# Kernel tuning notes

Hardware: AMD Instinct MI355X
Metric: run time of the kernel (lower is better)

## Reference

```python
import jax, jax.numpy as jnp
import numpy as np

B, N, IN_C, OUT_C = 32, 1024, 64, 128
ALPHA = 0.2  # LeakyReLU negative slope
NEG_INF = -1e16


def setup_inputs() -> dict:
    key = jax.random.key(0)
    k1, k2, k3, k4, k5 = jax.random.split(key, 5)
    inputs = jax.random.normal(k1, (B, N, IN_C), dtype=jnp.float32)
    # dense 0/1 adjacency mask
    graph = jax.random.randint(k2, (N, N), 0, 2).astype(jnp.float32)
    # torch nn.Linear weight layout: [out_c, in_c]
    W = jax.random.normal(k3, (OUT_C, IN_C), dtype=jnp.float32)
    b = jax.random.normal(k4, (OUT_C,), dtype=jnp.float32)
    a = jax.random.normal(k5, (2 * OUT_C, 1), dtype=jnp.float32)
    return {"inputs": inputs, "graph": graph, "W": W, "b": b, "a": a}


def reference(inputs, graph, W, b, a):
    # h = W(inputs): [B, N, D]
    h = jnp.einsum('bnt,dt->bnd', inputs, W)
    # cat([h_i, h_j]) @ a  ==  h_i @ a1 + h_j @ a2  (decomposed, no [B,N,N,2D] tensor)
    a1 = a[:OUT_C, 0]   # [D]
    a2 = a[OUT_C:, 0]   # [D]
    s1 = jnp.einsum('bnd,d->bn', h, a1)  # score contribution of node i
    s2 = jnp.einsum('bnd,d->bn', h, a2)  # score contribution of node j
    e = s1[:, :, None] + s2[:, None, :]  # [B, N, N]
    e = jnp.where(e > 0, e, ALPHA * e)   # LeakyReLU
    e = e * graph                        # zero out non-edges
    # torch masked_fill_(eq(outputs, 0), -1e16)
    e = jnp.where(e == 0.0, NEG_INF, e)
    attention = jax.nn.softmax(e, axis=2)  # [B, N, N]
    out = jnp.einsum('bij,bjd->bid', attention, h) + b  # [B, N, D]
    return out
```

## Files before the change

kernel.cpp:

```cpp
#include <hip/hip_runtime.h>
#include <hip/hip_bf16.h>

#define ALPHA 0.2f

typedef unsigned short ushort_t;
typedef unsigned int   uint_t;
typedef unsigned short ushort8 __attribute__((ext_vector_type(8)));
typedef uint_t uintv4 __attribute__((ext_vector_type(4)));
typedef float f32x4 __attribute__((ext_vector_type(4)));
typedef __bf16 bf16x8 __attribute__((ext_vector_type(8)));

__device__ __forceinline__ ushort_t f2bf(float f) {
  unsigned u = __float_as_uint(f);
  u += 0x7fffu + ((u >> 16) & 1u);
  return (ushort_t)(u >> 16);
}

__global__ __launch_bounds__(256) void gat_pack_kernel(
    const float* __restrict__ graph, const float* __restrict__ W,
    const float* __restrict__ avec, uint_t* __restrict__ gmask,
    float* __restrict__ u)
{
  const int row = blockIdx.x, t = threadIdx.x;
  __shared__ uint_t nibs[256];
  float4 g = ((const float4*)(graph + (size_t)row * 1024))[t];
  uint_t nib = (g.x != 0.f ? 1u : 0u) | (g.y != 0.f ? 2u : 0u) |
               (g.z != 0.f ? 4u : 0u) | (g.w != 0.f ? 8u : 0u);
  nibs[t] = nib;
  __syncthreads();
  if (t < 32) {
    uint_t wd = 0;
#pragma unroll
    for (int k = 0; k < 8; ++k) wd |= nibs[t * 8 + k] << (4 * k);
    gmask[(size_t)row * 32 + t] = wd;
  }
  if (row == 0 && t < 128) {
    const int k  = t & 63;
    const int ao = (t >> 6) * 128;
    float a0 = 0.f, a1 = 0.f, a2 = 0.f, a3 = 0.f;
    for (int d = 0; d < 128; d += 4) {
      a0 = fmaf(avec[ao + d + 0], W[(d + 0) * 64 + k], a0);
      a1 = fmaf(avec[ao + d + 1], W[(d + 1) * 64 + k], a1);
      a2 = fmaf(avec[ao + d + 2], W[(d + 2) * 64 + k], a2);
      a3 = fmaf(avec[ao + d + 3], W[(d + 3) * 64 + k], a3);
    }
    u[t] = (a0 + a1) + (a2 + a3);
  }
}

__global__ __launch_bounds__(256) void gat_h_kernel(
    const float* __restrict__ inp, const float* __restrict__ W,
    const float* __restrict__ uvec, ushort_t* __restrict__ hT,
    float* __restrict__ s1, float* __restrict__ s2)
{
  const int b  = blockIdx.x >> 4;
  const int n0 = (blockIdx.x & 15) << 6;
  const int t  = threadIdx.x;
  const int d  = t & 127;
  const int nh = t >> 7;

  __shared__ float    x_lds[64][68];
  __shared__ float    u_lds[128];
  __shared__ ushort_t h_tile[128][72];

  float wreg[64];
  {
    const float4* wrow = (const float4*)(W + d * 64);
#pragma unroll
    for (int k = 0; k < 16; ++k) {
      float4 v = wrow[k];
      wreg[4*k+0] = v.x; wreg[4*k+1] = v.y; wreg[4*k+2] = v.z; wreg[4*k+3] = v.w;
    }
  }
  if (t < 128) u_lds[t] = uvec[t];

  {
    const float4* xsrc = (const float4*)(inp + ((size_t)b * 1024 + n0) * 64);
#pragma unroll
    for (int k = 0; k < 4; ++k) {
      const int g = k * 256 + t;
      const int n = g >> 4, c = g & 15;
      *(float4*)&x_lds[n][c * 4] = xsrc[g];
    }
  }
  __syncthreads();

  for (int r = 0; r < 32; ++r) {
    const int n = nh * 32 + r;
    const float* xr = &x_lds[n][0];
    float ax = 0.f, ay = 0.f, az = 0.f, aw = 0.f;
#pragma unroll
    for (int k = 0; k < 16; ++k) {
      float4 xv = *(const float4*)&xr[4 * k];
      ax = fmaf(wreg[4*k+0], xv.x, ax);
      ay = fmaf(wreg[4*k+1], xv.y, ay);
      az = fmaf(wreg[4*k+2], xv.z, az);
      aw = fmaf(wreg[4*k+3], xv.w, aw);
    }
    h_tile[d][n] = f2bf((ax + ay) + (az + aw));
  }

  if (t < 128) {
    const int n = t & 63, which = t >> 6;
    const float* xr = &x_lds[n][0];
    const float* uu = &u_lds[which * 64];
    float a0 = 0.f, a1 = 0.f, a2 = 0.f, a3 = 0.f;
#pragma unroll
    for (int k = 0; k < 16; ++k) {
      float4 xv = *(const float4*)&xr[4 * k];
      a0 = fmaf(xv.x, uu[4*k+0], a0);
      a1 = fmaf(xv.y, uu[4*k+1], a1);
      a2 = fmaf(xv.z, uu[4*k+2], a2);
      a3 = fmaf(xv.w, uu[4*k+3], a3);
    }
    const float sv = (a0 + a1) + (a2 + a3);
    if (which == 0) s1[(size_t)b * 1024 + n0 + n] = sv;
    else            s2[(size_t)b * 1024 + n0 + n] = sv;
  }
  __syncthreads();

#pragma unroll
  for (int it = 0; it < 4; ++it) {
    const int d2 = it * 32 + (t >> 3);
    const int ch = (t & 7) * 8;
    ushort8 v = *(const ushort8*)&h_tile[d2][ch];
    *(ushort8*)(hT + ((size_t)b * 128 + d2) * 1024 + n0 + ch) = v;
  }
}

__global__ __launch_bounds__(256) void gat_attn_kernel(
    const uint_t* __restrict__ gmask, const ushort_t* __restrict__ hT,
    const float* __restrict__ s1g, const float* __restrict__ s2g,
    const float* __restrict__ bias, float* __restrict__ out)
{
  const int ic = blockIdx.x;
  const int b  = blockIdx.y;
  const int i0 = ic << 6;
  const int t  = threadIdx.x;
  const int w  = t >> 6;
  const int l  = t & 63;
  const int ih = w >> 1;
  const int dh = w & 1;
  const int rlo = l & 15, rhi = rlo + 16;
  const int js  = (l >> 4) * 8;

  __shared__ float  s2_lds[1024];
  __shared__ uint_t mask_lds[64][33];
  __shared__ float  red_part[64][4];
  __shared__ float  red_row[64];

  ((float4*)s2_lds)[t] = ((const float4*)(s2g + (size_t)b * 1024))[t];
  {
    const uint4* gsrc = (const uint4*)(gmask + (size_t)i0 * 32);
#pragma unroll
    for (int k2 = 0; k2 < 2; ++k2) {
      const int idx = t + k2 * 256;
      uint4 mv = gsrc[idx];
      const int mr = idx >> 3, mc = (idx & 7) * 4;
      mask_lds[mr][mc + 0] = mv.x; mask_lds[mr][mc + 1] = mv.y;
      mask_lds[mr][mc + 2] = mv.z; mask_lds[mr][mc + 3] = mv.w;
    }
  }
  __syncthreads();

  {
    const int irow = t >> 2, bo = (t & 3) * 8;
    float mx = -1e30f;
    for (int jt = 0; jt < 32; ++jt) {
      const uint_t wd = mask_lds[irow][jt] >> bo;
      const float4 sA = *(const float4*)(s2_lds + jt * 32 + bo);
      const float4 sB = *(const float4*)(s2_lds + jt * 32 + bo + 4);
      if (wd & 1u)   mx = fmaxf(mx, sA.x);
      if (wd & 2u)   mx = fmaxf(mx, sA.y);
      if (wd & 4u)   mx = fmaxf(mx, sA.z);
      if (wd & 8u)   mx = fmaxf(mx, sA.w);
      if (wd & 16u)  mx = fmaxf(mx, sB.x);
      if (wd & 32u)  mx = fmaxf(mx, sB.y);
      if (wd & 64u)  mx = fmaxf(mx, sB.z);
      if (wd & 128u) mx = fmaxf(mx, sB.w);
    }
    red_part[irow][t & 3] = mx;
  }
  __syncthreads();
  if (t < 64)
    red_row[t] = fmaxf(fmaxf(red_part[t][0], red_part[t][1]),
                       fmaxf(red_part[t][2], red_part[t][3]));
  __syncthreads();

  const int ib = ih * 32;
  const float s1lo = s1g[(size_t)b * 1024 + i0 + ib + rlo];
  const float s1hi = s1g[(size_t)b * 1024 + i0 + ib + rhi];
  const float tl = s1lo + red_row[ib + rlo];
  const float th = s1hi + red_row[ib + rhi];
  const float Milo = tl > 0.f ? tl : ALPHA * tl;
  const float Mihi = th > 0.f ? th : ALPHA * th;

  const ushort_t* hb =
      hT + (size_t)b * 128 * 1024 + (size_t)(dh * 64 + rlo) * 1024 + js;

  f32x4 c[2][4];
#pragma unroll
  for (int is = 0; is < 2; ++is)
#pragma unroll
    for (int ds = 0; ds < 4; ++ds) c[is][ds] = f32x4{0.f, 0.f, 0.f, 0.f};
  float den_lo = 0.f, den_hi = 0.f;

  ushort8 bv[4], nb[4];
#pragma unroll
  for (int ds = 0; ds < 4; ++ds)
    bv[ds] = *(const ushort8*)(hb + (size_t)ds * 16 * 1024);

#pragma unroll 4
  for (int jt = 0; jt < 32; ++jt) {
    const int j0 = jt * 32;
    const int jn = (jt + 1 < 32) ? j0 + 32 : j0;
#pragma unroll
    for (int ds = 0; ds < 4; ++ds)
      nb[ds] = *(const ushort8*)(hb + (size_t)ds * 16 * 1024 + jn);

    const uint_t wlo = mask_lds[ib + rlo][jt] >> js;
    const uint_t whi = mask_lds[ib + rhi][jt] >> js;
    const float4 sA = *(const float4*)(s2_lds + j0 + js);
    const float4 sB = *(const float4*)(s2_lds + j0 + js + 4);
    const float sv[8] = {sA.x, sA.y, sA.z, sA.w, sB.x, sB.y, sB.z, sB.w};
    float plo[8], phi[8];
#pragma unroll
    for (int e = 0; e < 8; ++e) {
      float te = s1lo + sv[e];
      float v  = fmaxf(te, ALPHA * te);
      plo[e] = (((wlo >> e) & 1u) && v != 0.f) ? __expf(v - Milo) : 0.f;
      te = s1hi + sv[e];
      v  = fmaxf(te, ALPHA * te);
      phi[e] = (((whi >> e) & 1u) && v != 0.f) ? __expf(v - Mihi) : 0.f;
    }
    uint_t pkl[4], pkh[4];
#pragma unroll
    for (int q = 0; q < 4; ++q) {
      asm("v_cvt_pk_bf16_f32 %0, %1, %2"
          : "=v"(pkl[q]) : "v"(plo[2 * q]), "v"(plo[2 * q + 1]));
      asm("v_cvt_pk_bf16_f32 %0, %1, %2"
          : "=v"(pkh[q]) : "v"(phi[2 * q]), "v"(phi[2 * q + 1]));
      den_lo += __uint_as_float(pkl[q] << 16) +
                __uint_as_float(pkl[q] & 0xffff0000u);
      den_hi += __uint_as_float(pkh[q] << 16) +
                __uint_as_float(pkh[q] & 0xffff0000u);
    }
    const bf16x8 av0 =
        __builtin_bit_cast(bf16x8, (uintv4){pkl[0], pkl[1], pkl[2], pkl[3]});
    const bf16x8 av1 =
        __builtin_bit_cast(bf16x8, (uintv4){pkh[0], pkh[1], pkh[2], pkh[3]});
#pragma unroll
    for (int ds = 0; ds < 4; ++ds) {
      const bf16x8 bvv = __builtin_bit_cast(bf16x8, bv[ds]);
      c[0][ds] = __builtin_amdgcn_mfma_f32_16x16x32_bf16(av0, bvv, c[0][ds], 0, 0, 0);
      c[1][ds] = __builtin_amdgcn_mfma_f32_16x16x32_bf16(av1, bvv, c[1][ds], 0, 0, 0);
    }
#pragma unroll
    for (int ds = 0; ds < 4; ++ds) bv[ds] = nb[ds];
  }

  den_lo += __shfl_xor(den_lo, 16); den_lo += __shfl_xor(den_lo, 32);
  den_hi += __shfl_xor(den_hi, 16); den_hi += __shfl_xor(den_hi, 32);

#pragma unroll
  for (int ds = 0; ds < 4; ++ds) {
    const int col = dh * 64 + ds * 16 + rlo;
    const float bc = bias[col];
#pragma unroll
    for (int is = 0; is < 2; ++is) {
#pragma unroll
      for (int r = 0; r < 4; ++r) {
        const int row  = ib + is * 16 + (l >> 4) * 4 + r;
        const int srcl = (l >> 4) * 4 + r;
        const float dr = is ? __shfl(den_hi, srcl) : __shfl(den_lo, srcl);
        const float val = dr > 0.f ? c[is][ds][r] / dr + bc : bc;
        out[((size_t)b * 1024 + i0 + row) * 128 + col] = val;
      }
    }
  }
}

extern "C" void kernel_launch(void* const* d_in, const int* in_sizes, int n_in,
                              void* d_out, int out_size, void* d_ws, size_t ws_size,
                              hipStream_t stream) {
  (void)in_sizes; (void)n_in; (void)out_size; (void)ws_size;
  const float* inp   = (const float*)d_in[0];
  const float* graph = (const float*)d_in[1];
  const float* W     = (const float*)d_in[2];
  const float* bias  = (const float*)d_in[3];
  const float* avec  = (const float*)d_in[4];
  float* out = (float*)d_out;

  char* ws = (char*)d_ws;
  ushort_t* hT = (ushort_t*)ws;
  float* s1    = (float*)(ws + (size_t)8 * 1024 * 1024);
  float* s2    = s1 + 32 * 1024;
  float* u     = s2 + 32 * 1024;
  uint_t* gm   = (uint_t*)(ws + (size_t)8 * 1024 * 1024 + 512 * 1024);

  gat_pack_kernel<<<1024, 256, 0, stream>>>(graph, W, avec, gm, u);
  gat_h_kernel<<<512, 256, 0, stream>>>(inp, W, u, hT, s1, s2);
  gat_attn_kernel<<<dim3(16, 32), 256, 0, stream>>>(gm, hT, s1, s2, bias, out);
}
```

Measured before the change: 74.75 us.

## Halve row tiles in h and attention kernels, add XCD-aware block swizzle

Both the h-projection and attention kernels now process 32 rows per block instead of 64, doubling grid size to 1024 blocks to better fill the GPU's compute units. The attention kernel moves to a 1D grid whose block-to-(batch, row-chunk) mapping interleaves batches across the low bits, so that blocks sharing a batch's hT land together for cache locality. Each wave now does one 16-row MFMA tile instead of two. In exchange, every loaded hT fragment feeds half as many MFMAs, so total hT traffic and per-block setup (s2 load, mask load, max reduction) double.

```diff
diff --git a/kernel.cpp b/kernel.cpp
--- a/kernel.cpp
+++ b/kernel.cpp
@@ -53,15 +53,15 @@
     const float* __restrict__ uvec, ushort_t* __restrict__ hT,
     float* __restrict__ s1, float* __restrict__ s2)
 {
-  const int b  = blockIdx.x >> 4;
-  const int n0 = (blockIdx.x & 15) << 6;
+  const int b  = blockIdx.x >> 5;
+  const int n0 = (blockIdx.x & 31) << 5;
   const int t  = threadIdx.x;
   const int d  = t & 127;
   const int nh = t >> 7;
 
-  __shared__ float    x_lds[64][68];
+  __shared__ float    x_lds[32][68];
   __shared__ float    u_lds[128];
-  __shared__ ushort_t h_tile[128][72];
+  __shared__ ushort_t h_tile[128][40];
 
   float wreg[64];
   {
@@ -77,7 +77,7 @@
   {
     const float4* xsrc = (const float4*)(inp + ((size_t)b * 1024 + n0) * 64);
 #pragma unroll
-    for (int k = 0; k < 4; ++k) {
+    for (int k = 0; k < 2; ++k) {
       const int g = k * 256 + t;
       const int n = g >> 4, c = g & 15;
       *(float4*)&x_lds[n][c * 4] = xsrc[g];
@@ -85,8 +85,8 @@
   }
   __syncthreads();
 
-  for (int r = 0; r < 32; ++r) {
-    const int n = nh * 32 + r;
+  for (int r = 0; r < 16; ++r) {
+    const int n = nh * 16 + r;
     const float* xr = &x_lds[n][0];
     float ax = 0.f, ay = 0.f, az = 0.f, aw = 0.f;
 #pragma unroll
@@ -100,8 +100,8 @@
     h_tile[d][n] = f2bf((ax + ay) + (az + aw));
   }
 
-  if (t < 128) {
-    const int n = t & 63, which = t >> 6;
+  if (t < 64) {
+    const int n = t & 31, which = t >> 5;
     const float* xr = &x_lds[n][0];
     const float* uu = &u_lds[which * 64];
     float a0 = 0.f, a1 = 0.f, a2 = 0.f, a3 = 0.f;
@@ -120,9 +120,10 @@
   __syncthreads();
 
 #pragma unroll
-  for (int it = 0; it < 4; ++it) {
-    const int d2 = it * 32 + (t >> 3);
-    const int ch = (t & 7) * 8;
+  for (int it = 0; it < 2; ++it) {
+    const int idx = it * 256 + t;
+    const int d2  = idx >> 2;
+    const int ch  = (idx & 3) * 8;
     ushort8 v = *(const ushort8*)&h_tile[d2][ch];
     *(ushort8*)(hT + ((size_t)b * 128 + d2) * 1024 + n0 + ch) = v;
   }
@@ -133,77 +134,66 @@
     const float* __restrict__ s1g, const float* __restrict__ s2g,
     const float* __restrict__ bias, float* __restrict__ out)
 {
-  const int ic = blockIdx.x;
-  const int b  = blockIdx.y;
-  const int i0 = ic << 6;
-  const int t  = threadIdx.x;
-  const int w  = t >> 6;
-  const int l  = t & 63;
-  const int ih = w >> 1;
-  const int dh = w & 1;
-  const int rlo = l & 15, rhi = rlo + 16;
+  const int bid = blockIdx.x;
+  const int b   = (bid & 7) * 4 + ((bid >> 3) >> 5);
+  const int ic  = (bid >> 3) & 31;
+  const int i0  = ic << 5;
+  const int t   = threadIdx.x;
+  const int w   = t >> 6;
+  const int l   = t & 63;
+  const int ih  = w >> 1;
+  const int dh  = w & 1;
+  const int rl  = l & 15;
   const int js  = (l >> 4) * 8;
 
   __shared__ float  s2_lds[1024];
-  __shared__ uint_t mask_lds[64][33];
-  __shared__ float  red_part[64][4];
-  __shared__ float  red_row[64];
+  __shared__ uint_t mask_lds[32][33];
+  __shared__ float  red_part[32][8];
+  __shared__ float  red_row[32];
 
   ((float4*)s2_lds)[t] = ((const float4*)(s2g + (size_t)b * 1024))[t];
   {
-    const uint4* gsrc = (const uint4*)(gmask + (size_t)i0 * 32);
-#pragma unroll
-    for (int k2 = 0; k2 < 2; ++k2) {
-      const int idx = t + k2 * 256;
-      uint4 mv = gsrc[idx];
-      const int mr = idx >> 3, mc = (idx & 7) * 4;
-      mask_lds[mr][mc + 0] = mv.x; mask_lds[mr][mc + 1] = mv.y;
-      mask_lds[mr][mc + 2] = mv.z; mask_lds[mr][mc + 3] = mv.w;
-    }
-  }
-  __syncthreads();
-
-  {
-    const int irow = t >> 2, bo = (t & 3) * 8;
+    uint4 mv = ((const uint4*)(gmask + (size_t)i0 * 32))[t];
+    const int mr = t >> 3, mc = (t & 7) * 4;
+    mask_lds[mr][mc + 0] = mv.x; mask_lds[mr][mc + 1] = mv.y;
+    mask_lds[mr][mc + 2] = mv.z; mask_lds[mr][mc + 3] = mv.w;
+  }
+  __syncthreads();
+
+  {
+    const int irow = t >> 3, bo = (t & 7) * 4;
     float mx = -1e30f;
     for (int jt = 0; jt < 32; ++jt) {
       const uint_t wd = mask_lds[irow][jt] >> bo;
       const float4 sA = *(const float4*)(s2_lds + jt * 32 + bo);
-      const float4 sB = *(const float4*)(s2_lds + jt * 32 + bo + 4);
-      if (wd & 1u)   mx = fmaxf(mx, sA.x);
-      if (wd & 2u)   mx = fmaxf(mx, sA.y);
-      if (wd & 4u)   mx = fmaxf(mx, sA.z);
-      if (wd & 8u)   mx = fmaxf(mx, sA.w);
-      if (wd & 16u)  mx = fmaxf(mx, sB.x);
-      if (wd & 32u)  mx = fmaxf(mx, sB.y);
-      if (wd & 64u)  mx = fmaxf(mx, sB.z);
-      if (wd & 128u) mx = fmaxf(mx, sB.w);
-    }
-    red_part[irow][t & 3] = mx;
-  }
-  __syncthreads();
-  if (t < 64)
-    red_row[t] = fmaxf(fmaxf(red_part[t][0], red_part[t][1]),
-                       fmaxf(red_part[t][2], red_part[t][3]));
-  __syncthreads();
-
-  const int ib = ih * 32;
-  const float s1lo = s1g[(size_t)b * 1024 + i0 + ib + rlo];
-  const float s1hi = s1g[(size_t)b * 1024 + i0 + ib + rhi];
-  const float tl = s1lo + red_row[ib + rlo];
-  const float th = s1hi + red_row[ib + rhi];
-  const float Milo = tl > 0.f ? tl : ALPHA * tl;
-  const float Mihi = th > 0.f ? th : ALPHA * th;
+      if (wd & 1u) mx = fmaxf(mx, sA.x);
+      if (wd & 2u) mx = fmaxf(mx, sA.y);
+      if (wd & 4u) mx = fmaxf(mx, sA.z);
+      if (wd & 8u) mx = fmaxf(mx, sA.w);
+    }
+    red_part[irow][t & 7] = mx;
+  }
+  __syncthreads();
+  if (t < 32) {
+    float m = red_part[t][0];
+#pragma unroll
+    for (int k = 1; k < 8; ++k) m = fmaxf(m, red_part[t][k]);
+    red_row[t] = m;
+  }
+  __syncthreads();
+
+  const int ib = ih * 16;
+  const float s1v = s1g[(size_t)b * 1024 + i0 + ib + rl];
+  const float tm  = s1v + red_row[ib + rl];
+  const float Mi  = tm > 0.f ? tm : ALPHA * tm;
 
   const ushort_t* hb =
-      hT + (size_t)b * 128 * 1024 + (size_t)(dh * 64 + rlo) * 1024 + js;
-
-  f32x4 c[2][4];
-#pragma unroll
-  for (int is = 0; is < 2; ++is)
-#pragma unroll
-    for (int ds = 0; ds < 4; ++ds) c[is][ds] = f32x4{0.f, 0.f, 0.f, 0.f};
-  float den_lo = 0.f, den_hi = 0.f;
+      hT + (size_t)b * 128 * 1024 + (size_t)(dh * 64 + rl) * 1024 + js;
+
+  f32x4 c[4];
+#pragma unroll
+  for (int ds = 0; ds < 4; ++ds) c[ds] = f32x4{0.f, 0.f, 0.f, 0.f};
+  float den = 0.f;
 
   ushort8 bv[4], nb[4];
 #pragma unroll
@@ -218,64 +208,50 @@
     for (int ds = 0; ds < 4; ++ds)
       nb[ds] = *(const ushort8*)(hb + (size_t)ds * 16 * 1024 + jn);
 
-    const uint_t wlo = mask_lds[ib + rlo][jt] >> js;
-    const uint_t whi = mask_lds[ib + rhi][jt] >> js;
+    const uint_t wd = mask_lds[ib + rl][jt] >> js;
     const float4 sA = *(const float4*)(s2_lds + j0 + js);
     const float4 sB = *(const float4*)(s2_lds + j0 + js + 4);
     const float sv[8] = {sA.x, sA.y, sA.z, sA.w, sB.x, sB.y, sB.z, sB.w};
-    float plo[8], phi[8];
+    float p[8];
 #pragma unroll
     for (int e = 0; e < 8; ++e) {
-      float te = s1lo + sv[e];
-      float v  = fmaxf(te, ALPHA * te);
-      plo[e] = (((wlo >> e) & 1u) && v != 0.f) ? __expf(v - Milo) : 0.f;
-      te = s1hi + sv[e];
-      v  = fmaxf(te, ALPHA * te);
-      phi[e] = (((whi >> e) & 1u) && v != 0.f) ? __expf(v - Mihi) : 0.f;
-    }
-    uint_t pkl[4], pkh[4];
+      const float te = s1v + sv[e];
+      const float v  = fmaxf(te, ALPHA * te);
+      p[e] = (((wd >> e) & 1u) && v != 0.f) ? __expf(v - Mi) : 0.f;
+    }
+    uint_t pk[4];
 #pragma unroll
     for (int q = 0; q < 4; ++q) {
       asm("v_cvt_pk_bf16_f32 %0, %1, %2"
-          : "=v"(pkl[q]) : "v"(plo[2 * q]), "v"(plo[2 * q + 1]));
-      asm("v_cvt_pk_bf16_f32 %0, %1, %2"
-          : "=v"(pkh[q]) : "v"(phi[2 * q]), "v"(phi[2 * q + 1]));
-      den_lo += __uint_as_float(pkl[q] << 16) +
-                __uint_as_float(pkl[q] & 0xffff0000u);
-      den_hi += __uint_as_float(pkh[q] << 16) +
-                __uint_as_float(pkh[q] & 0xffff0000u);
-    }
-    const bf16x8 av0 =
-        __builtin_bit_cast(bf16x8, (uintv4){pkl[0], pkl[1], pkl[2], pkl[3]});
-    const bf16x8 av1 =
-        __builtin_bit_cast(bf16x8, (uintv4){pkh[0], pkh[1], pkh[2], pkh[3]});
+          : "=v"(pk[q]) : "v"(p[2 * q]), "v"(p[2 * q + 1]));
+      den += __uint_as_float(pk[q] << 16) +
+             __uint_as_float(pk[q] & 0xffff0000u);
+    }
+    const bf16x8 av =
+        __builtin_bit_cast(bf16x8, (uintv4){pk[0], pk[1], pk[2], pk[3]});
 #pragma unroll
     for (int ds = 0; ds < 4; ++ds) {
       const bf16x8 bvv = __builtin_bit_cast(bf16x8, bv[ds]);
-      c[0][ds] = __builtin_amdgcn_mfma_f32_16x16x32_bf16(av0, bvv, c[0][ds], 0, 0, 0);
-      c[1][ds] = __builtin_amdgcn_mfma_f32_16x16x32_bf16(av1, bvv, c[1][ds], 0, 0, 0);
+      c[ds] = __builtin_amdgcn_mfma_f32_16x16x32_bf16(av, bvv, c[ds], 0, 0, 0);
     }
 #pragma unroll
     for (int ds = 0; ds < 4; ++ds) bv[ds] = nb[ds];
   }
 
-  den_lo += __shfl_xor(den_lo, 16); den_lo += __shfl_xor(den_lo, 32);
-  den_hi += __shfl_xor(den_hi, 16); den_hi += __shfl_xor(den_hi, 32);
+  den += __shfl_xor(den, 16);
+  den += __shfl_xor(den, 32);
 
 #pragma unroll
   for (int ds = 0; ds < 4; ++ds) {
-    const int col = dh * 64 + ds * 16 + rlo;
+    const int col = dh * 64 + ds * 16 + rl;
     const float bc = bias[col];
 #pragma unroll
-    for (int is = 0; is < 2; ++is) {
-#pragma unroll
-      for (int r = 0; r < 4; ++r) {
-        const int row  = ib + is * 16 + (l >> 4) * 4 + r;
-        const int srcl = (l >> 4) * 4 + r;
-        const float dr = is ? __shfl(den_hi, srcl) : __shfl(den_lo, srcl);
-        const float val = dr > 0.f ? c[is][ds][r] / dr + bc : bc;
-        out[((size_t)b * 1024 + i0 + row) * 128 + col] = val;
-      }
+    for (int r = 0; r < 4; ++r) {
+      const int rr   = (l >> 4) * 4 + r;
+      const int row  = ib + rr;
+      const float dr = __shfl(den, rr);
+      const float val = dr > 0.f ? c[ds][r] / dr + bc : bc;
+      out[((size_t)b * 1024 + i0 + row) * 128 + col] = val;
     }
   }
 }
@@ -299,6 +275,6 @@
   uint_t* gm   = (uint_t*)(ws + (size_t)8 * 1024 * 1024 + 512 * 1024);
 
   gat_pack_kernel<<<1024, 256, 0, stream>>>(graph, W, avec, gm, u);
-  gat_h_kernel<<<512, 256, 0, stream>>>(inp, W, u, hT, s1, s2);
-  gat_attn_kernel<<<dim3(16, 32), 256, 0, stream>>>(gm, hT, s1, s2, bias, out);
-}
+  gat_h_kernel<<<1024, 256, 0, stream>>>(inp, W, u, hT, s1, s2);
+  gat_attn_kernel<<<1024, 256, 0, stream>>>(gm, hT, s1, s2, bias, out);
+}
```

New measurement: 101.5 us. +35.8%, slower.

## Split attention j-range across waves with LDS reduction; halve h-kernel tile

Applied to the files above, without the earlier changes.

The attention kernel now gives each wave all 128 output columns for half of the j-range, instead of half the columns over the full j-range. Each softmax weight is therefore computed once rather than duplicated across two column halves. Partial accumulators and denominators from the second j-half are reduced through a new ~33KB LDS buffer. The MFMA block is bracketed with s_setprio, and the h kernel uses 32-node tiles to launch twice as many blocks. The trade-off is more LDS, which may reduce occupancy, plus higher register pressure from doubling the accumulators.

```diff
diff --git a/kernel.cpp b/kernel.cpp
--- a/kernel.cpp
+++ b/kernel.cpp
@@ -53,15 +53,15 @@
     const float* __restrict__ uvec, ushort_t* __restrict__ hT,
     float* __restrict__ s1, float* __restrict__ s2)
 {
-  const int b  = blockIdx.x >> 4;
-  const int n0 = (blockIdx.x & 15) << 6;
+  const int b  = blockIdx.x >> 5;
+  const int n0 = (blockIdx.x & 31) << 5;
   const int t  = threadIdx.x;
   const int d  = t & 127;
   const int nh = t >> 7;
 
-  __shared__ float    x_lds[64][68];
+  __shared__ float    x_lds[32][68];
   __shared__ float    u_lds[128];
-  __shared__ ushort_t h_tile[128][72];
+  __shared__ ushort_t h_tile[128][40];
 
   float wreg[64];
   {
@@ -77,7 +77,7 @@
   {
     const float4* xsrc = (const float4*)(inp + ((size_t)b * 1024 + n0) * 64);
 #pragma unroll
-    for (int k = 0; k < 4; ++k) {
+    for (int k = 0; k < 2; ++k) {
       const int g = k * 256 + t;
       const int n = g >> 4, c = g & 15;
       *(float4*)&x_lds[n][c * 4] = xsrc[g];
@@ -85,8 +85,8 @@
   }
   __syncthreads();
 
-  for (int r = 0; r < 32; ++r) {
-    const int n = nh * 32 + r;
+  for (int r = 0; r < 16; ++r) {
+    const int n = nh * 16 + r;
     const float* xr = &x_lds[n][0];
     float ax = 0.f, ay = 0.f, az = 0.f, aw = 0.f;
 #pragma unroll
@@ -100,8 +100,8 @@
     h_tile[d][n] = f2bf((ax + ay) + (az + aw));
   }
 
-  if (t < 128) {
-    const int n = t & 63, which = t >> 6;
+  if (t < 64) {
+    const int n = t & 31, which = t >> 5;
     const float* xr = &x_lds[n][0];
     const float* uu = &u_lds[which * 64];
     float a0 = 0.f, a1 = 0.f, a2 = 0.f, a3 = 0.f;
@@ -120,9 +120,10 @@
   __syncthreads();
 
 #pragma unroll
-  for (int it = 0; it < 4; ++it) {
-    const int d2 = it * 32 + (t >> 3);
-    const int ch = (t & 7) * 8;
+  for (int it = 0; it < 2; ++it) {
+    const int idx = it * 256 + t;
+    const int d2  = idx >> 2;
+    const int ch  = (idx & 3) * 8;
     ushort8 v = *(const ushort8*)&h_tile[d2][ch];
     *(ushort8*)(hT + ((size_t)b * 128 + d2) * 1024 + n0 + ch) = v;
   }
@@ -138,16 +139,18 @@
   const int i0 = ic << 6;
   const int t  = threadIdx.x;
   const int w  = t >> 6;
+  const int rg = w & 1;
+  const int jh = w >> 1;
   const int l  = t & 63;
-  const int ih = w >> 1;
-  const int dh = w & 1;
-  const int rlo = l & 15, rhi = rlo + 16;
-  const int js  = (l >> 4) * 8;
+  const int rl = l & 15;
+  const int js = (l >> 4) * 8;
 
   __shared__ float  s2_lds[1024];
   __shared__ uint_t mask_lds[64][33];
   __shared__ float  red_part[64][4];
   __shared__ float  red_row[64];
+  __shared__ float  credu[64][132];
+  __shared__ float  den_lds[64];
 
   ((float4*)s2_lds)[t] = ((const float4*)(s2g + (size_t)b * 1024))[t];
   {
@@ -187,41 +190,40 @@
                        fmaxf(red_part[t][2], red_part[t][3]));
   __syncthreads();
 
-  const int ib = ih * 32;
-  const float s1lo = s1g[(size_t)b * 1024 + i0 + ib + rlo];
-  const float s1hi = s1g[(size_t)b * 1024 + i0 + ib + rhi];
-  const float tl = s1lo + red_row[ib + rlo];
-  const float th = s1hi + red_row[ib + rhi];
+  const int ib = rg * 32;
+  const float s1lo = s1g[(size_t)b * 1024 + i0 + ib + rl];
+  const float s1hi = s1g[(size_t)b * 1024 + i0 + ib + 16 + rl];
+  const float tl = s1lo + red_row[ib + rl];
+  const float th = s1hi + red_row[ib + 16 + rl];
   const float Milo = tl > 0.f ? tl : ALPHA * tl;
   const float Mihi = th > 0.f ? th : ALPHA * th;
 
   const ushort_t* hb =
-      hT + (size_t)b * 128 * 1024 + (size_t)(dh * 64 + rlo) * 1024 + js;
-
-  f32x4 c[2][4];
+      hT + (size_t)b * 128 * 1024 + (size_t)rl * 1024 + jh * 512 + js;
+
+  f32x4 c[2][8];
 #pragma unroll
   for (int is = 0; is < 2; ++is)
 #pragma unroll
-    for (int ds = 0; ds < 4; ++ds) c[is][ds] = f32x4{0.f, 0.f, 0.f, 0.f};
+    for (int ds = 0; ds < 8; ++ds) c[is][ds] = f32x4{0.f, 0.f, 0.f, 0.f};
   float den_lo = 0.f, den_hi = 0.f;
 
-  ushort8 bv[4], nb[4];
-#pragma unroll
-  for (int ds = 0; ds < 4; ++ds)
+  ushort8 bv[8], nb[8];
+#pragma unroll
+  for (int ds = 0; ds < 8; ++ds)
     bv[ds] = *(const ushort8*)(hb + (size_t)ds * 16 * 1024);
 
-#pragma unroll 4
-  for (int jt = 0; jt < 32; ++jt) {
+  for (int jt = 0; jt < 16; ++jt) {
     const int j0 = jt * 32;
-    const int jn = (jt + 1 < 32) ? j0 + 32 : j0;
-#pragma unroll
-    for (int ds = 0; ds < 4; ++ds)
+    const int jn = (jt + 1 < 16) ? j0 + 32 : j0;
+#pragma unroll
+    for (int ds = 0; ds < 8; ++ds)
       nb[ds] = *(const ushort8*)(hb + (size_t)ds * 16 * 1024 + jn);
 
-    const uint_t wlo = mask_lds[ib + rlo][jt] >> js;
-    const uint_t whi = mask_lds[ib + rhi][jt] >> js;
-    const float4 sA = *(const float4*)(s2_lds + j0 + js);
-    const float4 sB = *(const float4*)(s2_lds + j0 + js + 4);
+    const uint_t wlo = mask_lds[ib + rl][jh * 16 + jt] >> js;
+    const uint_t whi = mask_lds[ib + 16 + rl][jh * 16 + jt] >> js;
+    const float4 sA = *(const float4*)(s2_lds + jh * 512 + j0 + js);
+    const float4 sB = *(const float4*)(s2_lds + jh * 512 + j0 + js + 4);
     const float sv[8] = {sA.x, sA.y, sA.z, sA.w, sB.x, sB.y, sB.z, sB.w};
     float plo[8], phi[8];
 #pragma unroll
@@ -249,32 +251,54 @@
         __builtin_bit_cast(bf16x8, (uintv4){pkl[0], pkl[1], pkl[2], pkl[3]});
     const bf16x8 av1 =
         __builtin_bit_cast(bf16x8, (uintv4){pkh[0], pkh[1], pkh[2], pkh[3]});
-#pragma unroll
-    for (int ds = 0; ds < 4; ++ds) {
+    __builtin_amdgcn_s_setprio(1);
+#pragma unroll
+    for (int ds = 0; ds < 8; ++ds) {
       const bf16x8 bvv = __builtin_bit_cast(bf16x8, bv[ds]);
       c[0][ds] = __builtin_amdgcn_mfma_f32_16x16x32_bf16(av0, bvv, c[0][ds], 0, 0, 0);
       c[1][ds] = __builtin_amdgcn_mfma_f32_16x16x32_bf16(av1, bvv, c[1][ds], 0, 0, 0);
     }
-#pragma unroll
-    for (int ds = 0; ds < 4; ++ds) bv[ds] = nb[ds];
+    __builtin_amdgcn_s_setprio(0);
+#pragma unroll
+    for (int ds = 0; ds < 8; ++ds) bv[ds] = nb[ds];
   }
 
   den_lo += __shfl_xor(den_lo, 16); den_lo += __shfl_xor(den_lo, 32);
   den_hi += __shfl_xor(den_hi, 16); den_hi += __shfl_xor(den_hi, 32);
 
-#pragma unroll
-  for (int ds = 0; ds < 4; ++ds) {
-    const int col = dh * 64 + ds * 16 + rlo;
-    const float bc = bias[col];
-#pragma unroll
-    for (int is = 0; is < 2; ++is) {
-#pragma unroll
-      for (int r = 0; r < 4; ++r) {
-        const int row  = ib + is * 16 + (l >> 4) * 4 + r;
-        const int srcl = (l >> 4) * 4 + r;
-        const float dr = is ? __shfl(den_hi, srcl) : __shfl(den_lo, srcl);
-        const float val = dr > 0.f ? c[is][ds][r] / dr + bc : bc;
-        out[((size_t)b * 1024 + i0 + row) * 128 + col] = val;
+  if (jh == 1) {
+#pragma unroll
+    for (int is = 0; is < 2; ++is)
+#pragma unroll
+      for (int ds = 0; ds < 8; ++ds)
+#pragma unroll
+        for (int r = 0; r < 4; ++r)
+          credu[ib + is * 16 + (l >> 4) * 4 + r][ds * 16 + rl] = c[is][ds][r];
+    if (l < 16) {
+      den_lds[ib + rl]      = den_lo;
+      den_lds[ib + 16 + rl] = den_hi;
+    }
+  }
+  __syncthreads();
+  if (jh == 0) {
+    const float dl = den_lo + den_lds[ib + rl];
+    const float dh = den_hi + den_lds[ib + 16 + rl];
+    const float inv_lo = dl > 0.f ? 1.f / dl : 0.f;
+    const float inv_hi = dh > 0.f ? 1.f / dh : 0.f;
+#pragma unroll
+    for (int ds = 0; ds < 8; ++ds) {
+      const int col = ds * 16 + rl;
+      const float bc = bias[col];
+#pragma unroll
+      for (int is = 0; is < 2; ++is) {
+#pragma unroll
+        for (int r = 0; r < 4; ++r) {
+          const int rr  = (l >> 4) * 4 + r;
+          const int row = ib + is * 16 + rr;
+          const float cc = c[is][ds][r] + credu[row][col];
+          const float iv = __shfl(is ? inv_hi : inv_lo, rr);
+          out[((size_t)b * 1024 + i0 + row) * 128 + col] = fmaf(cc, iv, bc);
+        }
       }
     }
   }
@@ -299,6 +323,6 @@
   uint_t* gm   = (uint_t*)(ws + (size_t)8 * 1024 * 1024 + 512 * 1024);
 
   gat_pack_kernel<<<1024, 256, 0, stream>>>(graph, W, avec, gm, u);
-  gat_h_kernel<<<512, 256, 0, stream>>>(inp, W, u, hT, s1, s2);
+  gat_h_kernel<<<1024, 256, 0, stream>>>(inp, W, u, hT, s1, s2);
   gat_attn_kernel<<<dim3(16, 32), 256, 0, stream>>>(gm, hT, s1, s2, bias, out);
 }
```

Result: no change. 75.40 us (+0.9%).
